# Kernel tuning notes

Hardware: AMD Instinct MI355X
Metric: run time of the kernel (lower is better)

Reference implementation:

```python
import jax, jax.numpy as jnp
import numpy as np

N_NODES = 50000
N_EDGES = 800000
IN_DIM = 128
HID = 64
HEADS = 2
OUT_DIM = 2
N_GRAPHS = 512
NEG_SLOPE = 0.2


def setup_inputs() -> dict:
    key = jax.random.key(0)
    ks = jax.random.split(key, 16)
    x = jax.random.normal(ks[0], (N_NODES, IN_DIM), dtype=jnp.float32)
    edge_index = jax.random.randint(ks[1], (2, N_EDGES), 0, N_NODES, dtype=jnp.int64)
    batch = jnp.sort(jax.random.randint(ks[2], (N_NODES,), 0, N_GRAPHS, dtype=jnp.int64))
    s = 0.1
    W1 = jax.random.normal(ks[3], (IN_DIM, HEADS * HID), dtype=jnp.float32) * s
    a_src1 = jax.random.normal(ks[4], (HEADS, HID), dtype=jnp.float32) * s
    a_dst1 = jax.random.normal(ks[5], (HEADS, HID), dtype=jnp.float32) * s
    b1 = jnp.zeros((HEADS * HID,), dtype=jnp.float32)
    W2 = jax.random.normal(ks[6], (HEADS * HID, HID), dtype=jnp.float32) * s
    a_src2 = jax.random.normal(ks[7], (1, HID), dtype=jnp.float32) * s
    a_dst2 = jax.random.normal(ks[8], (1, HID), dtype=jnp.float32) * s
    b2 = jnp.zeros((HID,), dtype=jnp.float32)
    fcW = jax.random.normal(ks[9], (HID, OUT_DIM), dtype=jnp.float32) * s
    fcb = jnp.zeros((OUT_DIM,), dtype=jnp.float32)
    return dict(x=x, edge_index=edge_index, batch=batch,
                W1=W1, a_src1=a_src1, a_dst1=a_dst1, b1=b1,
                W2=W2, a_src2=a_src2, a_dst2=a_dst2, b2=b2,
                fcW=fcW, fcb=fcb)


def gat_layer(x, src, dst, W, a_src, a_dst, b, heads, c_out):
    # x: [N, F] -> h: [N, H, C]
    N = x.shape[0]
    h = (x @ W).reshape(N, heads, c_out)
    alpha_s = jnp.sum(h * a_src, axis=-1)  # [N, H]
    alpha_d = jnp.sum(h * a_dst, axis=-1)  # [N, H]
    e = jax.nn.leaky_relu(alpha_s[src] + alpha_d[dst], NEG_SLOPE)  # [E, H]
    # segment softmax over destination nodes
    emax = jax.ops.segment_max(e, dst, num_segments=N)  # [N, H]
    ex = jnp.exp(e - emax[dst])
    denom = jax.ops.segment_sum(ex, dst, num_segments=N)  # [N, H]
    coef = ex / denom[dst]  # [E, H]
    msg = h[src] * coef[..., None]  # [E, H, C]
    out = jax.ops.segment_sum(msg, dst, num_segments=N)  # [N, H, C]
    return out.reshape(N, heads * c_out) + b


def reference(x, edge_index, batch, W1, a_src1, a_dst1, b1, W2, a_src2, a_dst2, b2, fcW, fcb):
    N = x.shape[0]
    # PyG GATConv add_self_loops=True (shared graph for both layers)
    loops = jnp.arange(N, dtype=edge_index.dtype)
    src = jnp.concatenate([edge_index[0], loops])
    dst = jnp.concatenate([edge_index[1], loops])
    h = jax.nn.relu(gat_layer(x, src, dst, W1, a_src1, a_dst1, b1, HEADS, HID))
    h = jax.nn.relu(gat_layer(h, src, dst, W2, a_src2, a_dst2, b2, 1, HID))
    # global mean pool over graphs
    sums = jax.ops.segment_sum(h, batch, num_segments=N_GRAPHS)  # [G, HID]
    cnts = jax.ops.segment_sum(jnp.ones((N,), dtype=h.dtype), batch, num_segments=N_GRAPHS)
    pooled = sums / jnp.maximum(cnts, 1.0)[:, None]
    logits = pooled @ fcW + fcb
    return jax.nn.log_softmax(logits, axis=1)
```

## Files before the change

kernel.cpp:

```cpp
#include <hip/hip_runtime.h>
#include <math.h>

#define N_NODES 50000
#define N_EDGES 800000
#define EP (N_EDGES + N_NODES)
#define IN_DIM 128
#define HID 64
#define HEADS 2
#define OUT_DIM 2
#define N_GRAPHS 512
#define NEG_SLOPE 0.2f
#define NB_SCAN 196

typedef unsigned int uint;
typedef unsigned short ushort;

__device__ __forceinline__ ushort f2bf(float f) {
    uint u = __float_as_uint(f);
    u += 0x7fffu + ((u >> 16) & 1u);
    return (ushort)(u >> 16);
}
__device__ __forceinline__ float bf_lo(uint u) { return __uint_as_float(u << 16); }
__device__ __forceinline__ float bf_hi(uint u) { return __uint_as_float(u & 0xffff0000u); }

__global__ void hist_kernel(const int* __restrict__ ei, int* __restrict__ cnt) {
    int i = blockIdx.x * blockDim.x + threadIdx.x;
    if (i >= EP) return;
    int d = (i < N_EDGES) ? ei[N_EDGES + i] : (i - N_EDGES);
    atomicAdd(&cnt[d], 1);
}

__global__ void partial_kernel(const int* __restrict__ cnt, int* __restrict__ bsum) {
    int tid = threadIdx.x;
    int i = blockIdx.x * 256 + tid;
    int lane = tid & 63, wid = tid >> 6;
    int v = (i < N_NODES) ? cnt[i] : 0;
#pragma unroll
    for (int off = 32; off; off >>= 1) v += __shfl_xor(v, off);
    __shared__ int wsum[4];
    if (lane == 0) wsum[wid] = v;
    __syncthreads();
    if (tid == 0) bsum[blockIdx.x] = wsum[0] + wsum[1] + wsum[2] + wsum[3];
}

__global__ void scanb_kernel(const int* __restrict__ bsum, int* __restrict__ boff,
                             int* __restrict__ rowptr) {
    int tid = threadIdx.x;
    int lane = tid & 63, wid = tid >> 6;
    int v = (tid < NB_SCAN) ? bsum[tid] : 0;
    int incl = v;
#pragma unroll
    for (int off = 1; off < 64; off <<= 1) {
        int t = __shfl_up(incl, off);
        if (lane >= off) incl += t;
    }
    __shared__ int wt[4];
    if (lane == 63) wt[wid] = incl;
    __syncthreads();
    int add = 0;
    for (int w = 0; w < wid; w++) add += wt[w];
    incl += add;
    if (tid < NB_SCAN) boff[tid] = incl - v;
    if (tid == NB_SCAN - 1) rowptr[N_NODES] = incl;
}

__global__ void scanc_kernel(const int* __restrict__ cnt, const int* __restrict__ boff,
                             int* __restrict__ rowptr, int* __restrict__ cursor) {
    int tid = threadIdx.x;
    int i = blockIdx.x * 256 + tid;
    int lane = tid & 63, wid = tid >> 6;
    int v = (i < N_NODES) ? cnt[i] : 0;
    int incl = v;
#pragma unroll
    for (int off = 1; off < 64; off <<= 1) {
        int t = __shfl_up(incl, off);
        if (lane >= off) incl += t;
    }
    __shared__ int wt[4];
    if (lane == 63) wt[wid] = incl;
    __syncthreads();
    int add = boff[blockIdx.x];
    for (int w = 0; w < wid; w++) add += wt[w];
    int excl = add + incl - v;
    if (i < N_NODES) { rowptr[i] = excl; cursor[i] = excl; }
}

__global__ void scatter_kernel(const int* __restrict__ ei, int* __restrict__ cursor,
                               int* __restrict__ csr_src) {
    int i = blockIdx.x * blockDim.x + threadIdx.x;
    if (i >= EP) return;
    int s, d;
    if (i < N_EDGES) { s = ei[i]; d = ei[N_EDGES + i]; }
    else             { s = d = i - N_EDGES; }
    int pos = atomicAdd(&cursor[d], 1);
    csr_src[pos] = s;
}

template<int K, int COLS, int NPB, int H>
__global__ void gemm_alphas(const float* __restrict__ X, const float* __restrict__ W,
                            ushort* __restrict__ Y,
                            const float* __restrict__ a_src, const float* __restrict__ a_dst,
                            float* __restrict__ as, float* __restrict__ ad, int n_nodes) {
    __shared__ float xs[NPB][K];
    const int base = blockIdx.x * NPB;
    const int tid = threadIdx.x;
    const int lane = tid & 63, wid = tid >> 6;
    const float4* X4 = (const float4*)X;
    for (int idx = tid; idx < NPB * (K / 4); idx += COLS) {
        int r = idx / (K / 4), c = idx % (K / 4);
        int n = base + r;
        float4 v = (n < n_nodes) ? X4[(size_t)n * (K / 4) + c] : make_float4(0.f, 0.f, 0.f, 0.f);
        ((float4*)xs[r])[c] = v;
    }
    __syncthreads();
    const float asv = a_src[wid * 64 + lane];
    const float adv = a_dst[wid * 64 + lane];
    float acc[NPB];
#pragma unroll
    for (int i = 0; i < NPB; i++) acc[i] = 0.f;
    for (int k = 0; k < K; k++) {
        float w = W[(size_t)k * COLS + tid];
#pragma unroll
        for (int i = 0; i < NPB; i++) acc[i] = fmaf(xs[i][k], w, acc[i]);
    }
#pragma unroll
    for (int i = 0; i < NPB; i++) {
        int n = base + i;
        if (n >= n_nodes) continue;
        Y[(size_t)n * COLS + tid] = f2bf(acc[i]);
        float s = acc[i] * asv;
        float d = acc[i] * adv;
#pragma unroll
        for (int off = 32; off; off >>= 1) {
            s += __shfl_xor(s, off);
            d += __shfl_xor(d, off);
        }
        if (lane == 0) {
            as[(size_t)n * H + wid] = s;
            ad[(size_t)n * H + wid] = d;
        }
    }
}

__device__ __forceinline__ float lrelu(float e) { return e > 0.f ? e : NEG_SLOPE * e; }

__global__ void node_agg1_kernel(const int* __restrict__ rowptr, const int* __restrict__ csr_src,
                                 const uint* __restrict__ Hb,
                                 const float* __restrict__ as, const float* __restrict__ ad,
                                 const float* __restrict__ b, float* __restrict__ outp) {
    int wave = threadIdx.x >> 6;
    int lane = threadIdx.x & 63;
    int node = blockIdx.x * 4 + wave;
    if (node >= N_NODES) return;
    const int lo = rowptr[node], hi = rowptr[node + 1];
    const float ad0 = ad[(size_t)node * 2 + 0], ad1 = ad[(size_t)node * 2 + 1];

    float exa0 = 0.f, exa1 = 0.f, exb0 = 0.f, exb1 = 0.f;
    int j1 = lo + lane;
    if (j1 < hi) {
        int s = csr_src[j1];
        float2 a = *(const float2*)&as[(size_t)s * 2];
        exa0 = __expf(lrelu(a.x + ad0));
        exa1 = __expf(lrelu(a.y + ad1));
    }
    int j2 = lo + 64 + lane;
    if (j2 < hi) {
        int s = csr_src[j2];
        float2 a = *(const float2*)&as[(size_t)s * 2];
        exb0 = __expf(lrelu(a.x + ad0));
        exb1 = __expf(lrelu(a.y + ad1));
    }
    float d0 = exa0 + exb0, d1 = exa1 + exb1;
    for (int j = lo + 128 + lane; j < hi; j += 64) {
        int s = csr_src[j];
        float2 a = *(const float2*)&as[(size_t)s * 2];
        d0 += __expf(lrelu(a.x + ad0));
        d1 += __expf(lrelu(a.y + ad1));
    }
#pragma unroll
    for (int off = 32; off; off >>= 1) {
        d0 += __shfl_xor(d0, off);
        d1 += __shfl_xor(d1, off);
    }
    const float inv = (lane < 32) ? (1.f / d0) : (1.f / d1);
    const bool h0side = (lane < 32);

    float acc0 = 0.f, acc1 = 0.f;
    const int deg = hi - lo;
    const int n1 = deg < 64 ? deg : 64;
    int j = 0;
    for (; j + 4 <= n1; j += 4) {
        int s0 = csr_src[lo + j + 0], s1 = csr_src[lo + j + 1];
        int s2 = csr_src[lo + j + 2], s3 = csr_src[lo + j + 3];
        float ca0 = __shfl(exa0, j + 0), cb0 = __shfl(exa1, j + 0);
        float ca1 = __shfl(exa0, j + 1), cb1 = __shfl(exa1, j + 1);
        float ca2 = __shfl(exa0, j + 2), cb2 = __shfl(exa1, j + 2);
        float ca3 = __shfl(exa0, j + 3), cb3 = __shfl(exa1, j + 3);
        float c0 = h0side ? ca0 : cb0;
        float c1 = h0side ? ca1 : cb1;
        float c2 = h0side ? ca2 : cb2;
        float c3 = h0side ? ca3 : cb3;
        uint u0 = Hb[(size_t)s0 * 64 + lane];
        uint u1 = Hb[(size_t)s1 * 64 + lane];
        uint u2 = Hb[(size_t)s2 * 64 + lane];
        uint u3 = Hb[(size_t)s3 * 64 + lane];
        acc0 = fmaf(bf_lo(u0), c0, acc0); acc1 = fmaf(bf_hi(u0), c0, acc1);
        acc0 = fmaf(bf_lo(u1), c1, acc0); acc1 = fmaf(bf_hi(u1), c1, acc1);
        acc0 = fmaf(bf_lo(u2), c2, acc0); acc1 = fmaf(bf_hi(u2), c2, acc1);
        acc0 = fmaf(bf_lo(u3), c3, acc0); acc1 = fmaf(bf_hi(u3), c3, acc1);
    }
    for (; j < n1; j++) {
        int s = csr_src[lo + j];
        float ca = __shfl(exa0, j), cb = __shfl(exa1, j);
        float c = h0side ? ca : cb;
        uint u = Hb[(size_t)s * 64 + lane];
        acc0 = fmaf(bf_lo(u), c, acc0);
        acc1 = fmaf(bf_hi(u), c, acc1);
    }
    if (deg > 64) {
        const int n2 = deg < 128 ? deg : 128;
        for (j = 64; j < n2; j++) {
            int s = csr_src[lo + j];
            float ca = __shfl(exb0, j - 64), cb = __shfl(exb1, j - 64);
            float c = h0side ? ca : cb;
            uint u = Hb[(size_t)s * 64 + lane];
            acc0 = fmaf(bf_lo(u), c, acc0);
            acc1 = fmaf(bf_hi(u), c, acc1);
        }
        for (int jj = lo + 128; jj < hi; jj++) {
            int s = csr_src[jj];
            float2 a = *(const float2*)&as[(size_t)s * 2];
            float e0 = __expf(lrelu(a.x + ad0));
            float e1 = __expf(lrelu(a.y + ad1));
            float c = h0side ? e0 : e1;
            uint u = Hb[(size_t)s * 64 + lane];
            acc0 = fmaf(bf_lo(u), c, acc0);
            acc1 = fmaf(bf_hi(u), c, acc1);
        }
    }
    float v0 = acc0 * inv + b[2 * lane];
    float v1 = acc1 * inv + b[2 * lane + 1];
    v0 = v0 > 0.f ? v0 : 0.f;
    v1 = v1 > 0.f ? v1 : 0.f;
    *(float2*)&outp[(size_t)node * 128 + 2 * lane] = make_float2(v0, v1);
}

__global__ void node_agg2_kernel(const int* __restrict__ rowptr, const int* __restrict__ csr_src,
                                 const ushort* __restrict__ Hb,
                                 const float* __restrict__ as, const float* __restrict__ ad,
                                 const float* __restrict__ b, float* __restrict__ outp) {
    int wave = threadIdx.x >> 6;
    int lane = threadIdx.x & 63;
    int node = blockIdx.x * 4 + wave;
    if (node >= N_NODES) return;
    const int lo = rowptr[node], hi = rowptr[node + 1];
    const float adN = ad[node];

    float exa = 0.f, exb = 0.f;
    int j1 = lo + lane;
    if (j1 < hi) exa = __expf(lrelu(as[csr_src[j1]] + adN));
    int j2 = lo + 64 + lane;
    if (j2 < hi) exb = __expf(lrelu(as[csr_src[j2]] + adN));
    float d = exa + exb;
    for (int j = lo + 128 + lane; j < hi; j += 64)
        d += __expf(lrelu(as[csr_src[j]] + adN));
#pragma unroll
    for (int off = 32; off; off >>= 1) d += __shfl_xor(d, off);
    const float inv = 1.f / d;

    float acc = 0.f;
    const int deg = hi - lo;
    const int n1 = deg < 64 ? deg : 64;
    int j = 0;
    for (; j + 4 <= n1; j += 4) {
        int s0 = csr_src[lo + j + 0], s1 = csr_src[lo + j + 1];
        int s2 = csr_src[lo + j + 2], s3 = csr_src[lo + j + 3];
        float c0 = __shfl(exa, j + 0), c1 = __shfl(exa, j + 1);
        float c2 = __shfl(exa, j + 2), c3 = __shfl(exa, j + 3);
        float h0 = __uint_as_float(((uint)Hb[(size_t)s0 * 64 + lane]) << 16);
        float h1 = __uint_as_float(((uint)Hb[(size_t)s1 * 64 + lane]) << 16);
        float h2 = __uint_as_float(((uint)Hb[(size_t)s2 * 64 + lane]) << 16);
        float h3 = __uint_as_float(((uint)Hb[(size_t)s3 * 64 + lane]) << 16);
        acc = fmaf(h0, c0, acc);
        acc = fmaf(h1, c1, acc);
        acc = fmaf(h2, c2, acc);
        acc = fmaf(h3, c3, acc);
    }
    for (; j < n1; j++) {
        float c = __shfl(exa, j);
        acc = fmaf(__uint_as_float(((uint)Hb[(size_t)csr_src[lo + j] * 64 + lane]) << 16), c, acc);
    }
    if (deg > 64) {
        const int n2 = deg < 128 ? deg : 128;
        for (j = 64; j < n2; j++) {
            float c = __shfl(exb, j - 64);
            acc = fmaf(__uint_as_float(((uint)Hb[(size_t)csr_src[lo + j] * 64 + lane]) << 16), c, acc);
        }
        for (int jj = lo + 128; jj < hi; jj++) {
            int s = csr_src[jj];
            float c = __expf(lrelu(as[s] + adN));
            acc = fmaf(__uint_as_float(((uint)Hb[(size_t)s * 64 + lane]) << 16), c, acc);
        }
    }
    float v = acc * inv + b[lane];
    outp[(size_t)node * 64 + lane] = v > 0.f ? v : 0.f;
}

__global__ void pool_fc_kernel(const float* __restrict__ act2,
                               const int* __restrict__ batch,
                               const float* __restrict__ fcW,
                               const float* __restrict__ fcb,
                               float* __restrict__ out) {
    int g = blockIdx.x;
    int tid = threadIdx.x;
    int wid = tid >> 6, c = tid & 63;
    __shared__ int slo, shi;
    if (tid == 0) {
        int lo = 0, hi = N_NODES;
        while (lo < hi) { int m = (lo + hi) >> 1; if (batch[m] < g) lo = m + 1; else hi = m; }
        slo = lo;
        lo = 0; hi = N_NODES;
        while (lo < hi) { int m = (lo + hi) >> 1; if (batch[m] < g + 1) lo = m + 1; else hi = m; }
        shi = lo;
    }
    __syncthreads();
    const int lo = slo, hi = shi;
    float sum = 0.f;
    for (int n = lo + wid; n < hi; n += 4) sum += act2[(size_t)n * HID + c];
    __shared__ float ps[4][HID];
    ps[wid][c] = sum;
    __syncthreads();
    if (wid == 0) {
        float t = ps[0][c] + ps[1][c] + ps[2][c] + ps[3][c];
        float cnt = (float)(hi - lo);
        __shared__ float pooled[HID];
        pooled[c] = t / fmaxf(cnt, 1.f);
        __syncthreads();
        __shared__ float ls[OUT_DIM];
        if (c < OUT_DIM) {
            float l = fcb[c];
#pragma unroll 8
            for (int k = 0; k < HID; k++) l = fmaf(pooled[k], fcW[k * OUT_DIM + c], l);
            ls[c] = l;
        }
        __syncthreads();
        if (c < OUT_DIM) {
            float m = fmaxf(ls[0], ls[1]);
            float lse = m + logf(expf(ls[0] - m) + expf(ls[1] - m));
            out[(size_t)g * OUT_DIM + c] = ls[c] - lse;
        }
    }
}

extern "C" void kernel_launch(void* const* d_in, const int* in_sizes, int n_in,
                              void* d_out, int out_size, void* d_ws, size_t ws_size,
                              hipStream_t stream) {
    const float* x    = (const float*)d_in[0];
    const int*   ei   = (const int*)d_in[1];
    const int*   batch= (const int*)d_in[2];
    const float* W1   = (const float*)d_in[3];
    const float* as1w = (const float*)d_in[4];
    const float* ad1w = (const float*)d_in[5];
    const float* b1   = (const float*)d_in[6];
    const float* W2   = (const float*)d_in[7];
    const float* as2w = (const float*)d_in[8];
    const float* ad2w = (const float*)d_in[9];
    const float* b2   = (const float*)d_in[10];
    const float* fcW  = (const float*)d_in[11];
    const float* fcb  = (const float*)d_in[12];

    const size_t N = N_NODES;
    float* ws = (float*)d_ws;
    ushort* h1b  = (ushort*)ws;
    float* act1  = ws + N * 64;
    ushort* h2b  = (ushort*)(act1 + N * 128);
    float* out2  = act1 + N * 128 + N * 32;
    float* alps1 = out2 + N * 64;
    float* alpd1 = alps1 + N * 2;
    float* alps2 = alpd1 + N * 2;
    float* alpd2 = alps2 + N;
    int* cnt     = (int*)(alpd2 + N);
    int* rowptr  = cnt + N;
    int* cursor  = rowptr + N + 1;
    int* bsum    = cursor + N;
    int* boff    = bsum + NB_SCAN;
    int* csr_src = boff + NB_SCAN;

    hipMemsetAsync(cnt, 0, N * sizeof(int), stream);
    hist_kernel<<<(EP + 255) / 256, 256, 0, stream>>>(ei, cnt);
    partial_kernel<<<NB_SCAN, 256, 0, stream>>>(cnt, bsum);
    scanb_kernel<<<1, 256, 0, stream>>>(bsum, boff, rowptr);
    scanc_kernel<<<NB_SCAN, 256, 0, stream>>>(cnt, boff, rowptr, cursor);
    scatter_kernel<<<(EP + 255) / 256, 256, 0, stream>>>(ei, cursor, csr_src);

    gemm_alphas<128, 128, 4, 2><<<(N + 3) / 4, 128, 0, stream>>>(
        x, W1, h1b, as1w, ad1w, alps1, alpd1, (int)N);
    node_agg1_kernel<<<(N + 3) / 4, 256, 0, stream>>>(
        rowptr, csr_src, (const uint*)h1b, alps1, alpd1, b1, act1);

    gemm_alphas<128, 64, 8, 1><<<(N + 7) / 8, 64, 0, stream>>>(
        act1, W2, h2b, as2w, ad2w, alps2, alpd2, (int)N);
    node_agg2_kernel<<<(N + 3) / 4, 256, 0, stream>>>(
        rowptr, csr_src, h2b, alps2, alpd2, b2, out2);

    pool_fc_kernel<<<N_GRAPHS, 256, 0, stream>>>(out2, batch, fcW, fcb, (float*)d_out);
}
```

Measured before the change: 351.1 us.

## Record edge ranks in histogram pass and re-tile the two GEMM+alpha kernels

The histogram kernel now stores each edge's atomic rank, so the scatter pass computes its CSR position as rowptr[d]+rank with no second atomic and no cursor array. The two dense projection kernels are rewritten with larger per-thread register tiles: layer 1 uses 64 threads handling two output columns over 8 nodes, and layer 2 handles two columns over 4 nodes with 32-lane reductions. Weight loads are unrolled by 4 and X is read from shared memory as float4, raising reuse per load. The cost is an extra EP-sized rank buffer write and read, plus more registers per thread.

```diff
diff --git a/kernel.cpp b/kernel.cpp
--- a/kernel.cpp
+++ b/kernel.cpp
@@ -23,11 +23,12 @@
 __device__ __forceinline__ float bf_lo(uint u) { return __uint_as_float(u << 16); }
 __device__ __forceinline__ float bf_hi(uint u) { return __uint_as_float(u & 0xffff0000u); }
 
-__global__ void hist_kernel(const int* __restrict__ ei, int* __restrict__ cnt) {
+__global__ void hist_kernel(const int* __restrict__ ei, int* __restrict__ cnt,
+                            int* __restrict__ erank) {
     int i = blockIdx.x * blockDim.x + threadIdx.x;
     if (i >= EP) return;
     int d = (i < N_EDGES) ? ei[N_EDGES + i] : (i - N_EDGES);
-    atomicAdd(&cnt[d], 1);
+    erank[i] = atomicAdd(&cnt[d], 1);
 }
 
 __global__ void partial_kernel(const int* __restrict__ cnt, int* __restrict__ bsum) {
@@ -65,7 +66,7 @@
 }
 
 __global__ void scanc_kernel(const int* __restrict__ cnt, const int* __restrict__ boff,
-                             int* __restrict__ rowptr, int* __restrict__ cursor) {
+                             int* __restrict__ rowptr) {
     int tid = threadIdx.x;
     int i = blockIdx.x * 256 + tid;
     int lane = tid & 63, wid = tid >> 6;
@@ -82,63 +83,134 @@
     int add = boff[blockIdx.x];
     for (int w = 0; w < wid; w++) add += wt[w];
     int excl = add + incl - v;
-    if (i < N_NODES) { rowptr[i] = excl; cursor[i] = excl; }
-}
-
-__global__ void scatter_kernel(const int* __restrict__ ei, int* __restrict__ cursor,
-                               int* __restrict__ csr_src) {
+    if (i < N_NODES) rowptr[i] = excl;
+}
+
+__global__ void scatter_kernel(const int* __restrict__ ei, const int* __restrict__ rowptr,
+                               const int* __restrict__ erank, int* __restrict__ csr_src) {
     int i = blockIdx.x * blockDim.x + threadIdx.x;
     if (i >= EP) return;
     int s, d;
     if (i < N_EDGES) { s = ei[i]; d = ei[N_EDGES + i]; }
     else             { s = d = i - N_EDGES; }
-    int pos = atomicAdd(&cursor[d], 1);
-    csr_src[pos] = s;
-}
-
-template<int K, int COLS, int NPB, int H>
-__global__ void gemm_alphas(const float* __restrict__ X, const float* __restrict__ W,
-                            ushort* __restrict__ Y,
-                            const float* __restrict__ a_src, const float* __restrict__ a_dst,
-                            float* __restrict__ as, float* __restrict__ ad, int n_nodes) {
-    __shared__ float xs[NPB][K];
-    const int base = blockIdx.x * NPB;
-    const int tid = threadIdx.x;
-    const int lane = tid & 63, wid = tid >> 6;
+    csr_src[rowptr[d] + erank[i]] = s;
+}
+
+__global__ void gemm_alphas1(const float* __restrict__ X, const float* __restrict__ W,
+                             ushort* __restrict__ Y,
+                             const float* __restrict__ a_src, const float* __restrict__ a_dst,
+                             float* __restrict__ as, float* __restrict__ ad, int n_nodes) {
+    __shared__ float xs[8][128];
+    const int base = blockIdx.x * 8;
+    const int t = threadIdx.x;
     const float4* X4 = (const float4*)X;
-    for (int idx = tid; idx < NPB * (K / 4); idx += COLS) {
-        int r = idx / (K / 4), c = idx % (K / 4);
+    for (int idx = t; idx < 8 * 32; idx += 64) {
+        int r = idx >> 5, c = idx & 31;
         int n = base + r;
-        float4 v = (n < n_nodes) ? X4[(size_t)n * (K / 4) + c] : make_float4(0.f, 0.f, 0.f, 0.f);
+        float4 v = (n < n_nodes) ? X4[(size_t)n * 32 + c] : make_float4(0.f, 0.f, 0.f, 0.f);
         ((float4*)xs[r])[c] = v;
     }
     __syncthreads();
-    const float asv = a_src[wid * 64 + lane];
-    const float adv = a_dst[wid * 64 + lane];
-    float acc[NPB];
-#pragma unroll
-    for (int i = 0; i < NPB; i++) acc[i] = 0.f;
-    for (int k = 0; k < K; k++) {
-        float w = W[(size_t)k * COLS + tid];
-#pragma unroll
-        for (int i = 0; i < NPB; i++) acc[i] = fmaf(xs[i][k], w, acc[i]);
-    }
-#pragma unroll
-    for (int i = 0; i < NPB; i++) {
+
+    float acc0[8], acc1[8];
+#pragma unroll
+    for (int i = 0; i < 8; i++) { acc0[i] = 0.f; acc1[i] = 0.f; }
+    for (int k = 0; k < 128; k += 4) {
+        float wA[4], wB[4];
+#pragma unroll
+        for (int kk = 0; kk < 4; kk++) {
+            wA[kk] = W[(size_t)(k + kk) * 128 + t];
+            wB[kk] = W[(size_t)(k + kk) * 128 + 64 + t];
+        }
+#pragma unroll
+        for (int i = 0; i < 8; i++) {
+            float4 xv = *(const float4*)&xs[i][k];
+            float xx0 = xv.x, xx1 = xv.y, xx2 = xv.z, xx3 = xv.w;
+            acc0[i] = fmaf(xx0, wA[0], acc0[i]); acc1[i] = fmaf(xx0, wB[0], acc1[i]);
+            acc0[i] = fmaf(xx1, wA[1], acc0[i]); acc1[i] = fmaf(xx1, wB[1], acc1[i]);
+            acc0[i] = fmaf(xx2, wA[2], acc0[i]); acc1[i] = fmaf(xx2, wB[2], acc1[i]);
+            acc0[i] = fmaf(xx3, wA[3], acc0[i]); acc1[i] = fmaf(xx3, wB[3], acc1[i]);
+        }
+    }
+
+    const float asv0 = a_src[t],      adv0 = a_dst[t];
+    const float asv1 = a_src[64 + t], adv1 = a_dst[64 + t];
+#pragma unroll
+    for (int i = 0; i < 8; i++) {
         int n = base + i;
         if (n >= n_nodes) continue;
-        Y[(size_t)n * COLS + tid] = f2bf(acc[i]);
-        float s = acc[i] * asv;
-        float d = acc[i] * adv;
+        Y[(size_t)n * 128 + t]      = f2bf(acc0[i]);
+        Y[(size_t)n * 128 + 64 + t] = f2bf(acc1[i]);
+        float s0 = acc0[i] * asv0, d0 = acc0[i] * adv0;
+        float s1 = acc1[i] * asv1, d1 = acc1[i] * adv1;
 #pragma unroll
         for (int off = 32; off; off >>= 1) {
+            s0 += __shfl_xor(s0, off);
+            d0 += __shfl_xor(d0, off);
+            s1 += __shfl_xor(s1, off);
+            d1 += __shfl_xor(d1, off);
+        }
+        if (t == 0) {
+            as[(size_t)n * 2 + 0] = s0; as[(size_t)n * 2 + 1] = s1;
+            ad[(size_t)n * 2 + 0] = d0; ad[(size_t)n * 2 + 1] = d1;
+        }
+    }
+}
+
+__global__ void gemm_alphas2(const float* __restrict__ X, const float* __restrict__ W,
+                             ushort* __restrict__ Y,
+                             const float* __restrict__ a_src, const float* __restrict__ a_dst,
+                             float* __restrict__ as, float* __restrict__ ad, int n_nodes) {
+    __shared__ float xs[8][128];
+    const int base = blockIdx.x * 8;
+    const int t = threadIdx.x;
+    const int g = t >> 5, c = t & 31;
+    const float4* X4 = (const float4*)X;
+    for (int idx = t; idx < 8 * 32; idx += 64) {
+        int r = idx >> 5, cc = idx & 31;
+        int n = base + r;
+        float4 v = (n < n_nodes) ? X4[(size_t)n * 32 + cc] : make_float4(0.f, 0.f, 0.f, 0.f);
+        ((float4*)xs[r])[cc] = v;
+    }
+    __syncthreads();
+
+    float acc0[4], acc1[4];
+#pragma unroll
+    for (int i = 0; i < 4; i++) { acc0[i] = 0.f; acc1[i] = 0.f; }
+    for (int k = 0; k < 128; k += 4) {
+        float wA[4], wB[4];
+#pragma unroll
+        for (int kk = 0; kk < 4; kk++) {
+            wA[kk] = W[(size_t)(k + kk) * 64 + c];
+            wB[kk] = W[(size_t)(k + kk) * 64 + 32 + c];
+        }
+#pragma unroll
+        for (int i = 0; i < 4; i++) {
+            float4 xv = *(const float4*)&xs[g * 4 + i][k];
+            float xx0 = xv.x, xx1 = xv.y, xx2 = xv.z, xx3 = xv.w;
+            acc0[i] = fmaf(xx0, wA[0], acc0[i]); acc1[i] = fmaf(xx0, wB[0], acc1[i]);
+            acc0[i] = fmaf(xx1, wA[1], acc0[i]); acc1[i] = fmaf(xx1, wB[1], acc1[i]);
+            acc0[i] = fmaf(xx2, wA[2], acc0[i]); acc1[i] = fmaf(xx2, wB[2], acc1[i]);
+            acc0[i] = fmaf(xx3, wA[3], acc0[i]); acc1[i] = fmaf(xx3, wB[3], acc1[i]);
+        }
+    }
+
+    const float asvA = a_src[c], asvB = a_src[32 + c];
+    const float advA = a_dst[c], advB = a_dst[32 + c];
+#pragma unroll
+    for (int i = 0; i < 4; i++) {
+        int n = base + g * 4 + i;
+        if (n >= n_nodes) continue;
+        Y[(size_t)n * 64 + c]      = f2bf(acc0[i]);
+        Y[(size_t)n * 64 + 32 + c] = f2bf(acc1[i]);
+        float s = acc0[i] * asvA + acc1[i] * asvB;
+        float d = acc0[i] * advA + acc1[i] * advB;
+#pragma unroll
+        for (int off = 16; off; off >>= 1) {
             s += __shfl_xor(s, off);
             d += __shfl_xor(d, off);
         }
-        if (lane == 0) {
-            as[(size_t)n * H + wid] = s;
-            ad[(size_t)n * H + wid] = d;
-        }
+        if (c == 0) { as[n] = s; ad[n] = d; }
     }
 }
 
@@ -381,24 +453,24 @@
     float* alpd2 = alps2 + N;
     int* cnt     = (int*)(alpd2 + N);
     int* rowptr  = cnt + N;
-    int* cursor  = rowptr + N + 1;
-    int* bsum    = cursor + N;
+    int* bsum    = rowptr + N + 1;
     int* boff    = bsum + NB_SCAN;
-    int* csr_src = boff + NB_SCAN;
+    int* erank   = boff + NB_SCAN;
+    int* csr_src = erank + EP;
 
     hipMemsetAsync(cnt, 0, N * sizeof(int), stream);
-    hist_kernel<<<(EP + 255) / 256, 256, 0, stream>>>(ei, cnt);
+    hist_kernel<<<(EP + 255) / 256, 256, 0, stream>>>(ei, cnt, erank);
     partial_kernel<<<NB_SCAN, 256, 0, stream>>>(cnt, bsum);
     scanb_kernel<<<1, 256, 0, stream>>>(bsum, boff, rowptr);
-    scanc_kernel<<<NB_SCAN, 256, 0, stream>>>(cnt, boff, rowptr, cursor);
-    scatter_kernel<<<(EP + 255) / 256, 256, 0, stream>>>(ei, cursor, csr_src);
-
-    gemm_alphas<128, 128, 4, 2><<<(N + 3) / 4, 128, 0, stream>>>(
+    scanc_kernel<<<NB_SCAN, 256, 0, stream>>>(cnt, boff, rowptr);
+    scatter_kernel<<<(EP + 255) / 256, 256, 0, stream>>>(ei, rowptr, erank, csr_src);
+
+    gemm_alphas1<<<(N + 7) / 8, 64, 0, stream>>>(
         x, W1, h1b, as1w, ad1w, alps1, alpd1, (int)N);
     node_agg1_kernel<<<(N + 3) / 4, 256, 0, stream>>>(
         rowptr, csr_src, (const uint*)h1b, alps1, alpd1, b1, act1);
 
-    gemm_alphas<128, 64, 8, 1><<<(N + 7) / 8, 64, 0, stream>>>(
+    gemm_alphas2<<<(N + 7) / 8, 64, 0, stream>>>(
         act1, W2, h2b, as2w, ad2w, alps2, alpd2, (int)N);
     node_agg2_kernel<<<(N + 3) / 4, 256, 0, stream>>>(
         rowptr, csr_src, h2b, alps2, alpd2, b2, out2);
```

Result: faster. 310.5 us (-11.6%).
